# Performance work log

Hardware: AMD Instinct MI355X
Metric: run time of the kernel (lower is better)

The kernel has to match this reference:

```python
import jax, jax.numpy as jnp
import numpy as np

SIZE = (4096, 4096)   # self.size
SIGMA = 1.0           # blur_sigma
NOISE_STD = 0.01      # noise_std


def _gauss_kernel(sigma):
    # scipy.ndimage.gaussian_filter: radius = int(truncate*sigma + 0.5), truncate=4.0
    r = int(4.0 * sigma + 0.5)
    x = np.arange(-r, r + 1, dtype=np.float32)
    k = np.exp(-0.5 * (x / sigma) ** 2)
    k = k / k.sum()
    return jnp.asarray(k), r


def _blur(img, sigma):
    # img: [C, H, W]; separable Gaussian, scipy mode='reflect' == jnp symmetric pad
    k, r = _gauss_kernel(sigma)
    x = jnp.pad(img, ((0, 0), (r, r), (r, r)), mode='symmetric')
    x = x[:, None]  # [C, 1, H+2r, W+2r] (NCHW)
    kh = k.reshape(1, 1, -1, 1)
    kw = k.reshape(1, 1, 1, -1)
    x = jax.lax.conv_general_dilated(x, kh, (1, 1), 'VALID')
    x = jax.lax.conv_general_dilated(x, kw, (1, 1), 'VALID')
    return x[:, 0]  # [C, H, W]


def setup_inputs() -> dict:
    key = jax.random.key(0)
    k1, k2 = jax.random.split(key)
    img = jax.random.normal(k1, (1, 2048, 2048), dtype=jnp.float32)
    noise = jax.random.normal(k2, (1,) + SIZE, dtype=jnp.float32)
    return {"img": img, "noise": noise}


def reference(img, noise):
    # bilinear resize, align_corners=False == jax half-pixel linear resize
    img = jax.image.resize(img, (img.shape[0],) + SIZE, method='linear')
    img = jnp.flip(img, axis=2)   # horizontal flip
    img = jnp.flip(img, axis=1)   # vertical flip
    img = jnp.rot90(img, k=1, axes=(1, 2))  # rot90, k fixed to 1
    img = img + noise * NOISE_STD
    img = _blur(img, SIGMA)
    img = jnp.log1p(jnp.clip(img, 0.0))  # clamp(min=0) then log1p
    return img
```

## Files before the change

kernel.cpp:

```cpp
#include <hip/hip_runtime.h>
#include <math.h>

#define N      4096
#define NIMG   2048
#define SPAN   128
#define TXN    120
#define HRW    16
#define PP     66
#define PR     68
#define IPOFF  (PR * PP)
#define NSX    35
#define NSY    64
#define NBLK   (NSX * NSY)

#define KW0 0.00013383063f
#define KW1 0.00443186160f
#define KW2 0.05399112800f
#define KW3 0.24197144000f
#define KW4 0.39894346870f

__device__ __forceinline__ int symi(int g) {
    g = (g < 0) ? (-1 - g) : g;
    g = (g >= N) ? (2 * N - 1 - g) : g;
    return g;
}

__device__ __forceinline__ void gload_lds4(const float* g, float* l) {
    __builtin_amdgcn_global_load_lds(
        (const __attribute__((address_space(1))) unsigned int*)g,
        (__attribute__((address_space(3))) unsigned int*)l, 4, 0, 0);
}

#define H9(A,B,C,D,E,F,G,H,I)                                                  \
    fmaf(KW0,(A), fmaf(KW1,(B), fmaf(KW2,(C), fmaf(KW3,(D), fmaf(KW4,(E),      \
    fmaf(KW3,(F), fmaf(KW2,(G), fmaf(KW1,(H), KW0*(I)))))))))

#define GCOL2(J, G) do {                                                       \
    const float p0_ = ipg[(J) - PP];                                           \
    const float p1_ = ipg[(J)];                                                \
    const float p2_ = ipg[(J) + PP];                                           \
    (G).x = fmaf(0.75f, p1_, 0.25f * p2_);                                     \
    (G).y = fmaf(0.25f, p0_, 0.75f * p1_);                                     \
} while (0)

#define PROD4(J2, D0, D1, D2, D3, Z0, Z1, Z2, Z3) do {                         \
    float2 gc_, gd_;                                                           \
    GCOL2((J2), gc_); GCOL2((J2) + 1, gd_);                                    \
    (D0).x = fmaf(0.25f, ga.x, fmaf(0.75f, gb.x, 0.01f * (Z0).x));             \
    (D0).y = fmaf(0.25f, ga.y, fmaf(0.75f, gb.y, 0.01f * (Z0).y));             \
    (D1).x = fmaf(0.75f, gb.x, fmaf(0.25f, gc_.x, 0.01f * (Z1).x));            \
    (D1).y = fmaf(0.75f, gb.y, fmaf(0.25f, gc_.y, 0.01f * (Z1).y));            \
    (D2).x = fmaf(0.25f, gb.x, fmaf(0.75f, gc_.x, 0.01f * (Z2).x));            \
    (D2).y = fmaf(0.25f, gb.y, fmaf(0.75f, gc_.y, 0.01f * (Z2).y));            \
    (D3).x = fmaf(0.75f, gc_.x, fmaf(0.25f, gd_.x, 0.01f * (Z3).x));           \
    (D3).y = fmaf(0.75f, gc_.y, fmaf(0.25f, gd_.y, 0.01f * (Z3).y));           \
    ga = gc_; gb = gd_;                                                        \
} while (0)

#define OUT1(K, GY) do {                                                       \
    float2 v_;                                                                 \
    v_.x = H9(win[K].x, win[K+1].x, win[K+2].x, win[K+3].x, win[K+4].x,        \
              win[K+5].x, win[K+6].x, win[K+7].x, win[K+8].x);                 \
    v_.y = H9(win[K].y, win[K+1].y, win[K+2].y, win[K+3].y, win[K+4].y,        \
              win[K+5].y, win[K+6].y, win[K+7].y, win[K+8].y);                 \
    float* sl_ = ((K) & 1) ? EX1 : EX0;                                        \
    *reinterpret_cast<float2*>(sl_ + 2 * lane) = v_;                           \
    const float2 l0_ = *reinterpret_cast<const float2*>(sl_ + oL0);            \
    const float2 l1_ = *reinterpret_cast<const float2*>(sl_ + oL1);            \
    const float2 r0_ = *reinterpret_cast<const float2*>(sl_ + oR0);            \
    const float2 r1_ = *reinterpret_cast<const float2*>(sl_ + oR1);            \
    float ox_ = KW0 * l0_.x; ox_ = fmaf(KW1, l0_.y, ox_);                      \
    ox_ = fmaf(KW2, l1_.x, ox_); ox_ = fmaf(KW3, l1_.y, ox_);                  \
    ox_ = fmaf(KW4, v_.x, ox_);  ox_ = fmaf(KW3, v_.y, ox_);                   \
    ox_ = fmaf(KW2, r0_.x, ox_); ox_ = fmaf(KW1, r0_.y, ox_);                  \
    ox_ = fmaf(KW0, r1_.x, ox_);                                               \
    float oy_ = KW0 * l0_.y; oy_ = fmaf(KW1, l1_.x, oy_);                      \
    oy_ = fmaf(KW2, l1_.y, oy_); oy_ = fmaf(KW3, v_.x, oy_);                   \
    oy_ = fmaf(KW4, v_.y, oy_);  oy_ = fmaf(KW3, r0_.x, oy_);                  \
    oy_ = fmaf(KW2, r0_.y, oy_); oy_ = fmaf(KW1, r1_.x, oy_);                  \
    oy_ = fmaf(KW0, r1_.y, oy_);                                               \
    float2 rr_;                                                                \
    rr_.x = __logf(1.0f + fmaxf(ox_, 0.0f));                                   \
    rr_.y = __logf(1.0f + fmaxf(oy_, 0.0f));                                   \
    if (okst) *reinterpret_cast<float2*>(out + (size_t)(GY) * N + gxs) = rr_;  \
} while (0)

#define SLIDE4() do {                                                          \
    _Pragma("unroll")                                                          \
    for (int i_ = 0; i_ < 8; ++i_) win[i_] = win[i_ + 4];                      \
} while (0)

__global__ __launch_bounds__(256, 6)
void TensorAugment_79216376807666_kernel(const float* __restrict__ img,
                                         const float* __restrict__ noise,
                                         float* __restrict__ out) {
    __shared__ __align__(16) float SH[IPOFF + 4 * 256];

    const int tid  = threadIdx.x;
    const int lane = tid & 63;
    const int wave = tid >> 6;

    float* const IP  = SH;
    float* const EX0 = SH + IPOFF + wave * 256;
    float* const EX1 = EX0 + 128;

    const int bid = blockIdx.x;
    int sx, sy;
    if (bid < 2 * NSY) { sy = bid >> 1; sx = (bid & 1) ? (NSX - 1) : 0; }
    else { const int t = bid - 2 * NSY; sx = 1 + t % (NSX - 2); sy = t / (NSX - 2); }
    const int x0 = sx * TXN;
    const int y0 = sy * 64;

    int gxa = x0 - 4, gxb = x0 + SPAN - 5;
    int mxa = symi(gxa), mxb = symi(gxb);
    int gxmin = min(mxa, mxb), gxmax = max(mxa, mxb);
    if (gxa <= 0) gxmin = 0;
    if (gxb >= N - 1) gxmax = N - 1;
    int umin = (N - 1) - gxmax, umax = (N - 1) - gxmin;
    int r0min = (umin - 1) >> 1;
    int r0max = (umax - 1) >> 1;
    int nrows = r0max - r0min + 2;

    int gya = y0 - 4, gyb = y0 + 67;
    int mya = symi(gya), myb = symi(gyb);
    int gymin = min(mya, myb), gymax = max(mya, myb);
    if (gya <= 0) gymin = 0;
    if (gyb >= N - 1) gymax = N - 1;
    int c0min = (gymin - 1) >> 1;
    (void)nrows;

    {
        const int gcol = min(max(c0min + lane, 0), NIMG - 1);
#pragma unroll
        for (int k = 0; k < 17; ++k) {
            const int r  = wave + 4 * k;
            const int ir = min(max(r0min + r, 0), NIMG - 1);
            gload_lds4(img + (size_t)ir * NIMG + gcol, IP + r * PP);
        }
    }

    const int y0w = y0 + HRW * wave;
    const int gxs = x0 - 4 + 2 * lane;
    const bool okst = (lane >= 2) && (lane <= 61) && (gxs <= N - 2);
    const bool yin  = (y0w >= 4) && (y0w + 19 <= N - 1);
    const bool xin  = (sx > 0) && (sx < NSX - 1);
    const bool fast = xin && yin;
    const int oL0 = max(2 * lane - 4, 0), oL1 = max(2 * lane - 2, 0);
    const int oR0 = min(2 * lane + 2, 126), oR1 = min(2 * lane + 4, 126);

    const int a    = (x0 >> 1) - 2 + lane;
    const int ipb  = (2047 - a - r0min) * PP;
    const float* const ipg = IP + ipb;
    const int jb   = ((y0w - 5) >> 1) - c0min;
    const float* const nzb = noise + ((size_t)(y0w - 4) * N + gxs);
#define LDNZ(DR) (*reinterpret_cast<const float2*>(nzb + (size_t)(DR) * N))

    float2 npre[12];
    if (fast) {
#pragma unroll
        for (int j = 0; j < 12; ++j) npre[j] = LDNZ(j);
    }

    __syncthreads();

    float2 win[12];

    if (fast) {
        float2 ga, gb;
        GCOL2(jb, ga);
        GCOL2(jb + 1, gb);

        PROD4(jb + 2, win[0], win[1], win[2],  win[3],  npre[0], npre[1], npre[2],  npre[3]);
        PROD4(jb + 4, win[4], win[5], win[6],  win[7],  npre[4], npre[5], npre[6],  npre[7]);
        PROD4(jb + 6, win[8], win[9], win[10], win[11], npre[8], npre[9], npre[10], npre[11]);

        {
            float2 n0 = LDNZ(12), n1 = LDNZ(13), n2 = LDNZ(14), n3 = LDNZ(15);
            OUT1(0, y0w + 0); OUT1(1, y0w + 1); OUT1(2, y0w + 2); OUT1(3, y0w + 3);
            SLIDE4();
            PROD4(jb + 8, win[8], win[9], win[10], win[11], n0, n1, n2, n3);
        }
        {
            float2 n0 = LDNZ(16), n1 = LDNZ(17), n2 = LDNZ(18), n3 = LDNZ(19);
            OUT1(0, y0w + 4); OUT1(1, y0w + 5); OUT1(2, y0w + 6); OUT1(3, y0w + 7);
            SLIDE4();
            PROD4(jb + 10, win[8], win[9], win[10], win[11], n0, n1, n2, n3);
        }
        {
            float2 n0 = LDNZ(20), n1 = LDNZ(21), n2 = LDNZ(22), n3 = LDNZ(23);
            OUT1(0, y0w + 8); OUT1(1, y0w + 9); OUT1(2, y0w + 10); OUT1(3, y0w + 11);
            SLIDE4();
            PROD4(jb + 12, win[8], win[9], win[10], win[11], n0, n1, n2, n3);
        }
        OUT1(0, y0w + 12); OUT1(1, y0w + 13); OUT1(2, y0w + 14); OUT1(3, y0w + 15);
    } else {
        const int gxm0 = symi(gxs), gxm1 = symi(gxs + 1);
        const int u0 = (N - 1) - gxm0, u1 = (N - 1) - gxm1;
        const int A0 = (((u0 - 1) >> 1) - r0min) * PP;
        const int A1 = (((u1 - 1) >> 1) - r0min) * PP;
        const float w10 = (u0 & 1) ? 0.25f : 0.75f, w00 = 1.0f - w10;
        const float w11 = (u1 & 1) ? 0.25f : 0.75f, w01 = 1.0f - w11;

        auto nzg = [&](int dr) -> float2 {
            const float* nr = noise + (size_t)symi(y0w - 4 + dr) * N;
            float2 r; r.x = nr[gxm0]; r.y = nr[gxm1]; return r;
        };
        auto dgen = [&](int dr, float2 nz) -> float2 {
            const int gym = symi(y0w - 4 + dr);
            const int jc  = ((gym - 1) >> 1) - c0min;
            const float wc1 = (gym & 1) ? 0.25f : 0.75f;
            const float wc0 = 1.0f - wc1;
            float2 r;
            {
                const float t = fmaf(wc0, IP[A0 + jc], wc1 * IP[A0 + jc + 1]);
                const float b = fmaf(wc0, IP[A0 + PP + jc], wc1 * IP[A0 + PP + jc + 1]);
                r.x = fmaf(w00, t, fmaf(w10, b, 0.01f * nz.x));
            }
            {
                const float t = fmaf(wc0, IP[A1 + jc], wc1 * IP[A1 + jc + 1]);
                const float b = fmaf(wc0, IP[A1 + PP + jc], wc1 * IP[A1 + PP + jc + 1]);
                r.y = fmaf(w01, t, fmaf(w11, b, 0.01f * nz.y));
            }
            return r;
        };

#pragma unroll
        for (int j = 0; j < 12; ++j) win[j] = dgen(j, nzg(j));

#pragma unroll
        for (int c = 0; c < 4; ++c) {
            float2 n0, n1, n2, n3;
            if (c < 3) { n0 = nzg(12 + 4 * c); n1 = nzg(13 + 4 * c);
                         n2 = nzg(14 + 4 * c); n3 = nzg(15 + 4 * c); }
            OUT1(0, y0w + 4 * c + 0); OUT1(1, y0w + 4 * c + 1);
            OUT1(2, y0w + 4 * c + 2); OUT1(3, y0w + 4 * c + 3);
            if (c < 3) {
                SLIDE4();
                win[8]  = dgen(12 + 4 * c, n0);
                win[9]  = dgen(13 + 4 * c, n1);
                win[10] = dgen(14 + 4 * c, n2);
                win[11] = dgen(15 + 4 * c, n3);
            }
        }
    }
#undef LDNZ
}

extern "C" void kernel_launch(void* const* d_in, const int* in_sizes, int n_in,
                              void* d_out, int out_size, void* d_ws, size_t ws_size,
                              hipStream_t stream) {
    const float* img   = (const float*)d_in[0];
    const float* noise = (const float*)d_in[1];
    float* out = (float*)d_out;

    dim3 grid(NBLK);
    TensorAugment_79216376807666_kernel<<<grid, 256, 0, stream>>>(img, noise, out);
}
```

Before: 144.0 us.

## Retile blocks as wide short strips with waves split across x

Changes block tiling from 128x64 tiles (waves stacked in y) to 480-wide by 16-tall strips where the four waves sit side by side in x. The staged source patch becomes 256 rows by 15 columns, loaded with plain global loads and LDS stores instead of direct global-to-LDS loads. The edge-block special ordering is dropped and occupancy is raised to 8 blocks per SM. The aim is less halo over-fetch per output, a smaller LDS footprint and higher occupancy. The trade-off is a column-strided image gather with poor coalescing and a different boundary and fast-path mix.

```diff
diff --git a/kernel.cpp b/kernel.cpp
--- a/kernel.cpp
+++ b/kernel.cpp
@@ -3,14 +3,15 @@
 
 #define N      4096
 #define NIMG   2048
-#define SPAN   128
-#define TXN    120
-#define HRW    16
-#define PP     66
-#define PR     68
-#define IPOFF  (PR * PP)
-#define NSX    35
-#define NSY    64
+#define TXW    120
+#define BXC    480
+#define BSPAN  488
+#define HRB    16
+#define PPI    15
+#define PR     256
+#define IPSZ   (PR * PPI)
+#define NSX    9
+#define NSY    256
 #define NBLK   (NSX * NSY)
 
 #define KW0 0.00013383063f
@@ -25,20 +26,14 @@
     return g;
 }
 
-__device__ __forceinline__ void gload_lds4(const float* g, float* l) {
-    __builtin_amdgcn_global_load_lds(
-        (const __attribute__((address_space(1))) unsigned int*)g,
-        (__attribute__((address_space(3))) unsigned int*)l, 4, 0, 0);
-}
-
 #define H9(A,B,C,D,E,F,G,H,I)                                                  \
     fmaf(KW0,(A), fmaf(KW1,(B), fmaf(KW2,(C), fmaf(KW3,(D), fmaf(KW4,(E),      \
     fmaf(KW3,(F), fmaf(KW2,(G), fmaf(KW1,(H), KW0*(I)))))))))
 
 #define GCOL2(J, G) do {                                                       \
-    const float p0_ = ipg[(J) - PP];                                           \
+    const float p0_ = ipg[(J) - PPI];                                          \
     const float p1_ = ipg[(J)];                                                \
-    const float p2_ = ipg[(J) + PP];                                           \
+    const float p2_ = ipg[(J) + PPI];                                          \
     (G).x = fmaf(0.75f, p1_, 0.25f * p2_);                                     \
     (G).y = fmaf(0.25f, p0_, 0.75f * p1_);                                     \
 } while (0)
@@ -90,28 +85,27 @@
     for (int i_ = 0; i_ < 8; ++i_) win[i_] = win[i_ + 4];                      \
 } while (0)
 
-__global__ __launch_bounds__(256, 6)
+__global__ __launch_bounds__(256, 8)
 void TensorAugment_79216376807666_kernel(const float* __restrict__ img,
                                          const float* __restrict__ noise,
                                          float* __restrict__ out) {
-    __shared__ __align__(16) float SH[IPOFF + 4 * 256];
+    __shared__ __align__(16) float SH[IPSZ + 4 * 256];
 
     const int tid  = threadIdx.x;
     const int lane = tid & 63;
     const int wave = tid >> 6;
 
     float* const IP  = SH;
-    float* const EX0 = SH + IPOFF + wave * 256;
+    float* const EX0 = SH + IPSZ + wave * 256;
     float* const EX1 = EX0 + 128;
 
     const int bid = blockIdx.x;
-    int sx, sy;
-    if (bid < 2 * NSY) { sy = bid >> 1; sx = (bid & 1) ? (NSX - 1) : 0; }
-    else { const int t = bid - 2 * NSY; sx = 1 + t % (NSX - 2); sy = t / (NSX - 2); }
-    const int x0 = sx * TXN;
-    const int y0 = sy * 64;
-
-    int gxa = x0 - 4, gxb = x0 + SPAN - 5;
+    const int sx  = bid % NSX;
+    const int sy  = bid / NSX;
+    const int x0  = sx * BXC;
+    const int y0  = sy * HRB;
+
+    int gxa = x0 - 4, gxb = x0 + BSPAN - 5;
     int mxa = symi(gxa), mxb = symi(gxb);
     int gxmin = min(mxa, mxb), gxmax = max(mxa, mxb);
     if (gxa <= 0) gxmin = 0;
@@ -121,7 +115,7 @@
     int r0max = (umax - 1) >> 1;
     int nrows = r0max - r0min + 2;
 
-    int gya = y0 - 4, gyb = y0 + 67;
+    int gya = y0 - 4, gyb = y0 + 19;
     int mya = symi(gya), myb = symi(gyb);
     int gymin = min(mya, myb), gymax = max(mya, myb);
     if (gya <= 0) gymin = 0;
@@ -130,29 +124,38 @@
     (void)nrows;
 
     {
-        const int gcol = min(max(c0min + lane, 0), NIMG - 1);
-#pragma unroll
-        for (int k = 0; k < 17; ++k) {
-            const int r  = wave + 4 * k;
+        const int srow = tid >> 2;
+        const int cq   = (tid & 3) * 4;
+#pragma unroll
+        for (int p = 0; p < 4; ++p) {
+            const int r  = srow + 64 * p;
             const int ir = min(max(r0min + r, 0), NIMG - 1);
-            gload_lds4(img + (size_t)ir * NIMG + gcol, IP + r * PP);
+            const float* src = img + (size_t)ir * NIMG;
+            float v0, v1, v2, v3;
+            v0 = src[min(max(c0min + cq + 0, 0), NIMG - 1)];
+            v1 = src[min(max(c0min + cq + 1, 0), NIMG - 1)];
+            v2 = src[min(max(c0min + cq + 2, 0), NIMG - 1)];
+            v3 = src[min(max(c0min + cq + 3, 0), NIMG - 1)];
+            float* dst = IP + r * PPI + cq;
+            dst[0] = v0; dst[1] = v1; dst[2] = v2;
+            if (cq < 12) dst[3] = v3;
         }
     }
 
-    const int y0w = y0 + HRW * wave;
-    const int gxs = x0 - 4 + 2 * lane;
+    const int x0w = x0 + TXW * wave;
+    const int gxs = x0w - 4 + 2 * lane;
     const bool okst = (lane >= 2) && (lane <= 61) && (gxs <= N - 2);
-    const bool yin  = (y0w >= 4) && (y0w + 19 <= N - 1);
-    const bool xin  = (sx > 0) && (sx < NSX - 1);
-    const bool fast = xin && yin;
+    const bool xinw = (x0w >= 4) && (x0w + 123 <= N - 1);
+    const bool yin  = (y0 >= 4) && (y0 + 19 <= N - 1);
+    const bool fast = xinw && yin;
     const int oL0 = max(2 * lane - 4, 0), oL1 = max(2 * lane - 2, 0);
     const int oR0 = min(2 * lane + 2, 126), oR1 = min(2 * lane + 4, 126);
 
-    const int a    = (x0 >> 1) - 2 + lane;
-    const int ipb  = (2047 - a - r0min) * PP;
+    const int a    = (x0w >> 1) - 2 + lane;
+    const int ipb  = (2047 - a - r0min) * PPI;
     const float* const ipg = IP + ipb;
-    const int jb   = ((y0w - 5) >> 1) - c0min;
-    const float* const nzb = noise + ((size_t)(y0w - 4) * N + gxs);
+    const int jb   = ((y0 - 5) >> 1) - c0min;
+    const float* const nzb = noise + ((size_t)(y0 - 4) * N + gxs);
 #define LDNZ(DR) (*reinterpret_cast<const float2*>(nzb + (size_t)(DR) * N))
 
     float2 npre[12];
@@ -176,49 +179,49 @@
 
         {
             float2 n0 = LDNZ(12), n1 = LDNZ(13), n2 = LDNZ(14), n3 = LDNZ(15);
-            OUT1(0, y0w + 0); OUT1(1, y0w + 1); OUT1(2, y0w + 2); OUT1(3, y0w + 3);
+            OUT1(0, y0 + 0); OUT1(1, y0 + 1); OUT1(2, y0 + 2); OUT1(3, y0 + 3);
             SLIDE4();
             PROD4(jb + 8, win[8], win[9], win[10], win[11], n0, n1, n2, n3);
         }
         {
             float2 n0 = LDNZ(16), n1 = LDNZ(17), n2 = LDNZ(18), n3 = LDNZ(19);
-            OUT1(0, y0w + 4); OUT1(1, y0w + 5); OUT1(2, y0w + 6); OUT1(3, y0w + 7);
+            OUT1(0, y0 + 4); OUT1(1, y0 + 5); OUT1(2, y0 + 6); OUT1(3, y0 + 7);
             SLIDE4();
             PROD4(jb + 10, win[8], win[9], win[10], win[11], n0, n1, n2, n3);
         }
         {
             float2 n0 = LDNZ(20), n1 = LDNZ(21), n2 = LDNZ(22), n3 = LDNZ(23);
-            OUT1(0, y0w + 8); OUT1(1, y0w + 9); OUT1(2, y0w + 10); OUT1(3, y0w + 11);
+            OUT1(0, y0 + 8); OUT1(1, y0 + 9); OUT1(2, y0 + 10); OUT1(3, y0 + 11);
             SLIDE4();
             PROD4(jb + 12, win[8], win[9], win[10], win[11], n0, n1, n2, n3);
         }
-        OUT1(0, y0w + 12); OUT1(1, y0w + 13); OUT1(2, y0w + 14); OUT1(3, y0w + 15);
+        OUT1(0, y0 + 12); OUT1(1, y0 + 13); OUT1(2, y0 + 14); OUT1(3, y0 + 15);
     } else {
         const int gxm0 = symi(gxs), gxm1 = symi(gxs + 1);
         const int u0 = (N - 1) - gxm0, u1 = (N - 1) - gxm1;
-        const int A0 = (((u0 - 1) >> 1) - r0min) * PP;
-        const int A1 = (((u1 - 1) >> 1) - r0min) * PP;
+        const int A0 = (((u0 - 1) >> 1) - r0min) * PPI;
+        const int A1 = (((u1 - 1) >> 1) - r0min) * PPI;
         const float w10 = (u0 & 1) ? 0.25f : 0.75f, w00 = 1.0f - w10;
         const float w11 = (u1 & 1) ? 0.25f : 0.75f, w01 = 1.0f - w11;
 
         auto nzg = [&](int dr) -> float2 {
-            const float* nr = noise + (size_t)symi(y0w - 4 + dr) * N;
+            const float* nr = noise + (size_t)symi(y0 - 4 + dr) * N;
             float2 r; r.x = nr[gxm0]; r.y = nr[gxm1]; return r;
         };
         auto dgen = [&](int dr, float2 nz) -> float2 {
-            const int gym = symi(y0w - 4 + dr);
+            const int gym = symi(y0 - 4 + dr);
             const int jc  = ((gym - 1) >> 1) - c0min;
             const float wc1 = (gym & 1) ? 0.25f : 0.75f;
             const float wc0 = 1.0f - wc1;
             float2 r;
             {
                 const float t = fmaf(wc0, IP[A0 + jc], wc1 * IP[A0 + jc + 1]);
-                const float b = fmaf(wc0, IP[A0 + PP + jc], wc1 * IP[A0 + PP + jc + 1]);
+                const float b = fmaf(wc0, IP[A0 + PPI + jc], wc1 * IP[A0 + PPI + jc + 1]);
                 r.x = fmaf(w00, t, fmaf(w10, b, 0.01f * nz.x));
             }
             {
                 const float t = fmaf(wc0, IP[A1 + jc], wc1 * IP[A1 + jc + 1]);
-                const float b = fmaf(wc0, IP[A1 + PP + jc], wc1 * IP[A1 + PP + jc + 1]);
+                const float b = fmaf(wc0, IP[A1 + PPI + jc], wc1 * IP[A1 + PPI + jc + 1]);
                 r.y = fmaf(w01, t, fmaf(w11, b, 0.01f * nz.y));
             }
             return r;
@@ -232,8 +235,8 @@
             float2 n0, n1, n2, n3;
             if (c < 3) { n0 = nzg(12 + 4 * c); n1 = nzg(13 + 4 * c);
                          n2 = nzg(14 + 4 * c); n3 = nzg(15 + 4 * c); }
-            OUT1(0, y0w + 4 * c + 0); OUT1(1, y0w + 4 * c + 1);
-            OUT1(2, y0w + 4 * c + 2); OUT1(3, y0w + 4 * c + 3);
+            OUT1(0, y0 + 4 * c + 0); OUT1(1, y0 + 4 * c + 1);
+            OUT1(2, y0 + 4 * c + 2); OUT1(3, y0 + 4 * c + 3);
             if (c < 3) {
                 SLIDE4();
                 win[8]  = dgen(12 + 4 * c, n0);
```

After: 168.0 us. 16.7% more time.
